# Kernel optimization log

Measured on AMD Instinct MI355X. Metric: run time of the kernel, lower is better.

The kernel has to match this reference:

```python
import jax, jax.numpy as jnp
import numpy as np
import math

B = 2
D_MODEL = 2048
L_MAX = 4096
FILTER_ORDER = 64
EMB_DIM = 3
SHORT_K = 3


def setup_inputs() -> dict:
    key = jax.random.key(0)
    ks = jax.random.split(key, 16)
    D = D_MODEL

    def n(k, shape, scale=0.02):
        return jax.random.normal(k, shape, dtype=jnp.float32) * scale

    return {
        "x": jax.random.normal(ks[0], (B, L_MAX, D), dtype=jnp.float32),
        "in_proj_w": n(ks[1], (3 * D, D)),
        "in_proj_b": n(ks[2], (3 * D,)),
        "short_w": n(ks[3], (3 * D, 1, SHORT_K), 0.3),   # depthwise conv weight (O, I/groups=1, K)
        "short_b": n(ks[4], (3 * D,), 0.1),
        "mlp_w0": n(ks[5], (FILTER_ORDER, EMB_DIM), 0.5),
        "mlp_b0": n(ks[6], (FILTER_ORDER,), 0.5),
        "sin_freq": jnp.ones((1, FILTER_ORDER), dtype=jnp.float32),  # Sin module, w=1, shared across MLP layers
        "mlp_w1": n(ks[7], (FILTER_ORDER, FILTER_ORDER), 0.1),
        "mlp_b1": n(ks[8], (FILTER_ORDER,), 0.1),
        "mlp_w2": n(ks[9], (FILTER_ORDER, FILTER_ORDER), 0.1),
        "mlp_b2": n(ks[10], (FILTER_ORDER,), 0.1),
        "mlp_w3": n(ks[11], (D, FILTER_ORDER), 0.1),      # final Linear(order -> d_model, bias=False)
        "filter_bias": jax.random.normal(ks[12], (D,), dtype=jnp.float32),  # HyenaFilter.bias ~ randn
        "out_proj_w": n(ks[13], (D, D)),
        "out_proj_b": n(ks[14], (D,)),
    }


def _pos_emb(L):
    # PositionalEmbedding: t in [0,1], 1 complex band (emb_dim=3 -> bands=1)
    t = jnp.linspace(0.0, 1.0, L)[:, None]               # (L, 1)
    t_resc = jnp.linspace(0.0, L - 1.0, L)
    w = 2.0 * math.pi * t_resc / L                       # (L,)
    bands = (EMB_DIM - 1) // 2
    f = jnp.linspace(1e-4, bands - 1.0, bands)           # (bands,)
    ang = f[None, :] * w[:, None]                        # (L, bands)
    # z = exp(-1j * f * w) -> real = cos, imag = -sin
    z = jnp.concatenate([t, jnp.cos(ang), -jnp.sin(ang)], axis=-1)  # (L, 3)
    return z, t


def _filter_k(L, w0, b0, freq, w1, b1, w2, b2, w3):
    z, t = _pos_emb(L)
    h = jnp.sin(freq * (z @ w0.T + b0))
    h = jnp.sin(freq * (h @ w1.T + b1))
    h = jnp.sin(freq * (h @ w2.T + b2))
    h = h @ w3.T                                         # (L, D)
    # ExponentialModulation: deltas = linspace(log(.01)/1.5, log(.01)/0.3, D)
    max_decay = math.log(0.01) / 0.3
    min_decay = math.log(0.01) / 1.5
    deltas = jnp.linspace(min_decay, max_decay, h.shape[-1])
    decay = jnp.exp(-t * jnp.abs(deltas)[None, :])       # (L, D)
    return (h * decay).T                                 # (D, L)


def _fftconv(u, k, bias):
    # fftconv_ref with gelu=False, no dropout_mask: u (B, D, L), k (D, L), bias (D,)
    L = u.shape[-1]
    n = 2 * L
    k_f = jnp.fft.rfft(k, n=n) / n                       # (D, L+1)
    u_f = jnp.fft.rfft(u, n=n)                           # (B, D, L+1)
    y = jnp.fft.irfft(u_f * k_f, n=n, norm="forward")[..., :L]
    return y + u * bias[:, None]


def reference(x, in_proj_w, in_proj_b, short_w, short_b, mlp_w0, mlp_b0, sin_freq,
              mlp_w1, mlp_b1, mlp_w2, mlp_b2, mlp_w3, filter_bias,
              out_proj_w, out_proj_b):
    Bn, L, D = x.shape
    u = x @ in_proj_w.T + in_proj_b                      # (B, L, 3D)
    u = jnp.transpose(u, (0, 2, 1))                      # (B, 3D, L)
    # depthwise short conv, padding = short_k - 1, truncate to L (causal-ish)
    uc = jax.lax.conv_general_dilated(
        u, short_w, window_strides=(1,),
        padding=[(SHORT_K - 1, SHORT_K - 1)],
        feature_group_count=3 * D,
        dimension_numbers=("NCH", "OIH", "NCH"))
    uc = uc[..., :L] + short_b[None, :, None]
    x0, x1, v = jnp.split(uc, 3, axis=1)                 # each (B, D, L)
    k = _filter_k(L, mlp_w0, mlp_b0, sin_freq, mlp_w1, mlp_b1, mlp_w2, mlp_b2, mlp_w3)
    # order=2 Hyena recurrence: single gated long-conv step
    v = v * x1
    v = _fftconv(v, k, filter_bias)
    y = v * x0                                           # (B, D, L)
    y = jnp.transpose(y, (0, 2, 1))                      # (B, L, D)
    return y @ out_proj_w.T + out_proj_b
```

## Files before the change

### kernel.cpp

```cpp
#include <hip/hip_runtime.h>
#include <hip/hip_bf16.h>
#include <cstdint>
#include <cstddef>

typedef __attribute__((ext_vector_type(8))) short    bf16x8;
typedef __attribute__((ext_vector_type(4))) float    f32x4;
typedef __attribute__((ext_vector_type(8))) unsigned short u16x8;
typedef __attribute__((ext_vector_type(4))) float    f32v4;
typedef __attribute__((ext_vector_type(4))) unsigned short u16v4;

__device__ __forceinline__ float b2f(unsigned short v) {
    return __builtin_bit_cast(float, ((unsigned int)v) << 16);
}
__device__ __forceinline__ unsigned short f2b(float f) {
    unsigned int u = __builtin_bit_cast(unsigned int, f);
    u += 0x7fffu + ((u >> 16) & 1u);
    return (unsigned short)(u >> 16);
}

__device__ __forceinline__ void async16(const void* g, void* l) {
    __builtin_amdgcn_global_load_lds(
        (const __attribute__((address_space(1))) unsigned int*)g,
        (__attribute__((address_space(3))) unsigned int*)l, 16, 0, 0);
}

__global__ __launch_bounds__(256) void cvt2_f32_bf16(
    const float* __restrict__ srcA, unsigned short* __restrict__ dstA, int n4A,
    const float* __restrict__ srcB, unsigned short* __restrict__ dstB, int n4B) {
    int i = blockIdx.x * blockDim.x + threadIdx.x;
    int stride = gridDim.x * blockDim.x;
    const int nTot = n4A + n4B;
    for (; i < nTot; i += stride) {
        const bool inA = (i < n4A);
        const f32v4* s4 = inA ? (const f32v4*)srcA : (const f32v4*)srcB;
        u16v4* d4 = inA ? (u16v4*)dstA : (u16v4*)dstB;
        const int k = inA ? i : (i - n4A);
        f32v4 v = s4[k];
        u16v4 o;
        o.x = f2b(v.x); o.y = f2b(v.y); o.z = f2b(v.z); o.w = f2b(v.w);
        d4[k] = o;
    }
}

__global__ __launch_bounds__(256) void cvt_f32_bf16(const float* __restrict__ src,
                                                    unsigned short* __restrict__ dst, int n4) {
    int i = blockIdx.x * blockDim.x + threadIdx.x;
    int stride = gridDim.x * blockDim.x;
    const f32v4* s4 = (const f32v4*)src;
    u16v4* d4 = (u16v4*)dst;
    for (; i < n4; i += stride) {
        f32v4 v = s4[i];
        u16v4 o;
        o.x = f2b(v.x); o.y = f2b(v.y); o.z = f2b(v.z); o.w = f2b(v.w);
        d4[i] = o;
    }
}

template <int MODE>
__global__ __launch_bounds__(512, 1) void gemm256(
    const unsigned short* __restrict__ A,
    const unsigned short* __restrict__ Bw,
    const float* __restrict__ bias,
    void* __restrict__ Cout,
    int M, int N, int K, int Lseq, int CH, int ntn)
{
    constexpr int SMEM_BYTES = (MODE == 1) ? 135168 : 131072;
    __shared__ char smemc[SMEM_BYTES];

    const int tid = threadIdx.x;
    const int w   = tid >> 6;
    const int l   = tid & 63;
    const int wm  = w & 1;
    const int wn  = w >> 1;
    const int quad = l >> 4;
    const int lq   = l & 15;

    const int bid = blockIdx.x;
    const int x  = bid & 7;
    const int j  = bid >> 3;
    const int bx = (j & 7) + 8 * (j >> 5);
    const int by = (x << 2) | ((j >> 3) & 3);
    const int n0 = bx * 256, m0 = by * 256;

    const int su0 = quad ^ (lq & 7);
    const int su1 = su0 ^ 4;

    uint32_t offAe[2][2], offBe[2][2];
    int dA[2][2], dB[2][2];
    #pragma unroll
    for (int h = 0; h < 2; ++h)
        #pragma unroll
        for (int c = 0; c < 2; ++c) {
            const int Lr = h * 128 + w * 16 + c * 8 + (l >> 3);
            const int gA = ((Lr & 64) << 1) | ((Lr & 128) >> 1) | (Lr & 63);
            const int u  = (l & 7) ^ (l >> 3);
            offAe[h][c] = (uint32_t)(m0 + gA) * (uint32_t)K + (uint32_t)(u * 8);
            offBe[h][c] = (uint32_t)(n0 + Lr) * (uint32_t)K + (uint32_t)(u * 8);
            const int rb = (h * 128 + w * 16 + c * 8) * 128;
            dA[h][c] = rb;
            dB[h][c] = 32768 + rb;
        }

#define STAGE_A(bs, h, tile) do { \
    async16(A + offAe[h][0] + (size_t)(tile) * 64, smemc + ((bs) * 65536 + dA[h][0])); \
    async16(A + offAe[h][1] + (size_t)(tile) * 64, smemc + ((bs) * 65536 + dA[h][1])); \
} while (0)
#define STAGE_B(bs, h, tile) do { \
    async16(Bw + offBe[h][0] + (size_t)(tile) * 64, smemc + ((bs) * 65536 + dB[h][0])); \
    async16(Bw + offBe[h][1] + (size_t)(tile) * 64, smemc + ((bs) * 65536 + dB[h][1])); \
} while (0)

    f32x4 acc[8][4] = {};
    bf16x8 bw[4][2], a[2][2];

#define LDB8(bs) do { \
    _Pragma("unroll") for (int jj = 0; jj < 4; ++jj) { \
        const int Lr = wn * 64 + jj * 16 + lq; \
        bw[jj][0] = *(const bf16x8*)(smemc + (bs) * 65536 + 32768 + Lr * 128 + su0 * 16); \
        bw[jj][1] = *(const bf16x8*)(smemc + (bs) * 65536 + 32768 + Lr * 128 + su1 * 16); \
    } } while (0)
#define LDA4(bs, q) do { \
    _Pragma("unroll") for (int mf = 0; mf < 2; ++mf) { \
        const int g = wm * 128 + (q) * 32 + mf * 16 + lq; \
        const int Lr = ((g & 64) << 1) | ((g & 128) >> 1) | (g & 63); \
        a[mf][0] = *(const bf16x8*)(smemc + (bs) * 65536 + Lr * 128 + su0 * 16); \
        a[mf][1] = *(const bf16x8*)(smemc + (bs) * 65536 + Lr * 128 + su1 * 16); \
    } } while (0)
#define MFMA16(q) do { \
    _Pragma("unroll") for (int mf = 0; mf < 2; ++mf) \
    _Pragma("unroll") for (int jj = 0; jj < 4; ++jj) \
    _Pragma("unroll") for (int kk = 0; kk < 2; ++kk) \
        acc[(q) * 2 + mf][jj] = __builtin_amdgcn_mfma_f32_16x16x32_bf16(a[mf][kk], bw[jj][kk], acc[(q) * 2 + mf][jj], 0, 0, 0); \
} while (0)
#define PHASE_SYNC() do { \
    __builtin_amdgcn_s_barrier(); \
    asm volatile("s_waitcnt lgkmcnt(0)" ::: "memory"); \
    __builtin_amdgcn_sched_barrier(0); \
    __builtin_amdgcn_s_setprio(1); \
} while (0)
#define PHASE_END() do { \
    __builtin_amdgcn_s_setprio(0); \
    __builtin_amdgcn_s_barrier(); \
} while (0)
#define PHASE_END_DRAIN(lastf) do { \
    __builtin_amdgcn_s_setprio(0); \
    if (lastf) asm volatile("s_waitcnt vmcnt(0)" ::: "memory"); \
    else       asm volatile("s_waitcnt vmcnt(6)" ::: "memory"); \
    __builtin_amdgcn_s_barrier(); \
} while (0)

    STAGE_B(0, 0, 0); STAGE_B(0, 1, 0); STAGE_A(0, 0, 0); STAGE_A(0, 1, 0);
    STAGE_B(1, 0, 1); STAGE_B(1, 1, 1); STAGE_A(1, 0, 1);
    asm volatile("s_waitcnt vmcnt(6)" ::: "memory");
    __builtin_amdgcn_s_barrier();

    const int nIt = K >> 7;
    for (int i = 0; i < nIt; ++i) {
        const bool last = (i == nIt - 1);
        const int t0 = 2 * i, t1 = 2 * i + 1;
        LDB8(0); LDA4(0, 0); STAGE_A(1, 1, t1);
        PHASE_SYNC(); MFMA16(0); PHASE_END();
        LDA4(0, 1); if (!last) STAGE_B(0, 0, t0 + 2);
        PHASE_SYNC(); MFMA16(1); PHASE_END();
        LDA4(0, 2); if (!last) STAGE_B(0, 1, t0 + 2);
        PHASE_SYNC(); MFMA16(2); PHASE_END();
        LDA4(0, 3); if (!last) STAGE_A(0, 0, t0 + 2);
        PHASE_SYNC(); MFMA16(3); PHASE_END_DRAIN(last);
        LDB8(1); LDA4(1, 0); if (!last) STAGE_A(0, 1, t0 + 2);
        PHASE_SYNC(); MFMA16(0); PHASE_END();
        LDA4(1, 1); if (!last) STAGE_B(1, 0, t1 + 2);
        PHASE_SYNC(); MFMA16(1); PHASE_END();
        LDA4(1, 2); if (!last) STAGE_B(1, 1, t1 + 2);
        PHASE_SYNC(); MFMA16(2); PHASE_END();
        LDA4(1, 3); if (!last) STAGE_A(1, 0, t1 + 2);
        PHASE_SYNC(); MFMA16(3); PHASE_END_DRAIN(last);
    }

    if (MODE == 0) {
        float* out = (float*)Cout;
        #pragma unroll
        for (int jj = 0; jj < 4; ++jj) {
            const int col = n0 + wn * 64 + jj * 16 + lq;
            const float bv = bias[col];
            #pragma unroll
            for (int i8 = 0; i8 < 8; ++i8) {
                const int rowb = m0 + wm * 128 + i8 * 16 + quad * 4;
                f32x4 c = acc[i8][jj];
                out[(size_t)(rowb + 0) * N + col] = c.x + bv;
                out[(size_t)(rowb + 1) * N + col] = c.y + bv;
                out[(size_t)(rowb + 2) * N + col] = c.z + bv;
                out[(size_t)(rowb + 3) * N + col] = c.w + bv;
            }
        }
    } else {
        unsigned short* sE = (unsigned short*)smemc;
        __syncthreads();
        #pragma unroll
        for (int jj = 0; jj < 4; ++jj) {
            const int nl = wn * 64 + jj * 16 + lq;
            const float bv = bias[n0 + nl];
            #pragma unroll
            for (int i8 = 0; i8 < 8; ++i8) {
                const int ml = wm * 128 + i8 * 16 + quad * 4;
                f32x4 c = acc[i8][jj];
                u16v4 pk;
                pk.x = f2b(c.x + bv); pk.y = f2b(c.y + bv);
                pk.z = f2b(c.z + bv); pk.w = f2b(c.w + bv);
                *(u16v4*)&sE[nl * 264 + ml] = pk;
            }
        }
        __syncthreads();
        unsigned short* uo = (unsigned short*)Cout;
        const int bI = m0 >> 12;
        const int l0 = m0 & 4095;
        for (int e = tid; e < 8192; e += 512) {
            const int nl = e >> 5, seg = e & 31;
            u16x8 v = *(const u16x8*)&sE[nl * 264 + seg * 8];
            *(u16x8*)&uo[(size_t)(bI * CH + n0 + nl) * Lseq + l0 + seg * 8] = v;
        }
    }
#undef STAGE_A
#undef STAGE_B
#undef LDB8
#undef LDA4
#undef MFMA16
#undef PHASE_SYNC
#undef PHASE_END
#undef PHASE_END_DRAIN
}

__global__ __launch_bounds__(256) void filter_kernel(
    const float* __restrict__ w0, const float* __restrict__ b0,
    const float* __restrict__ freq,
    const float* __restrict__ w1, const float* __restrict__ b1,
    const float* __restrict__ w2, const float* __restrict__ b2,
    const float* __restrict__ w3, float* __restrict__ kf)
{
    __shared__ float ha[64][64];
    __shared__ float hb[64][64];
    const int tid = threadIdx.x;
    const int l0 = blockIdx.x * 64;
    const int d0 = blockIdx.y * 256;
    const int l  = tid & 63;
    const int lg = l0 + l;
    const float tt = (float)lg * (1.0f / 4095.0f);
    const float wang = 6.283185307179586f * (float)lg * (1.0f / 4096.0f);
    const float a  = 1e-4f * wang;
    const float z0 = tt, z1 = cosf(a), z2 = -sinf(a);

    for (int e = tid; e < 4096; e += 256) {
        const int dim = e >> 6;
        float pre = z0 * w0[dim * 3] + z1 * w0[dim * 3 + 1] + z2 * w0[dim * 3 + 2] + b0[dim];
        ha[dim][l] = sinf(freq[dim] * pre);
    }
    __syncthreads();
    for (int e = tid; e < 4096; e += 256) {
        const int dim = e >> 6;
        float acc = b1[dim];
        #pragma unroll
        for (int jj = 0; jj < 64; ++jj) acc += w1[dim * 64 + jj] * ha[jj][l];
        hb[dim][l] = sinf(freq[dim] * acc);
    }
    __syncthreads();
    for (int e = tid; e < 4096; e += 256) {
        const int dim = e >> 6;
        float acc = b2[dim];
        #pragma unroll
        for (int jj = 0; jj < 64; ++jj) acc += w2[dim * 64 + jj] * hb[jj][l];
        ha[dim][l] = sinf(freq[dim] * acc);
    }
    __syncthreads();
    for (int d = d0 + (tid >> 6); d < d0 + 256; d += 4) {
        float acc = 0.f;
        #pragma unroll
        for (int jj = 0; jj < 64; ++jj) acc += w3[d * 64 + jj] * ha[jj][l];
        const float delta = fabsf(-3.0701134573253944f + (-5.999245642062483e-3f) * (float)d);
        kf[(size_t)d * 4096 + lg] = acc * __expf(-tt * delta);
    }
}

#define PIDX(i) ((i) + (((i) >> 5) << 2))

__device__ __forceinline__ void bfly_f(float& r1, float& i1, float& r2, float& i2, float wr, float wi) {
    float ur = r1, ui = i1, vr = r2, vi = i2;
    r1 = ur + vr; i1 = ui + vi;
    float dr = ur - vr, di = ui - vi;
    r2 = dr * wr - di * wi;
    i2 = dr * wi + di * wr;
}
__device__ __forceinline__ void bfly_i(float& r1, float& i1, float& r2, float& i2, float wr, float wi) {
    float vr = r2 * wr - i2 * wi, vi = r2 * wi + i2 * wr;
    float ur = r1, ui = i1;
    r1 = ur + vr; i1 = ui + vi;
    r2 = ur - vr; i2 = ui - vi;
}

template <int DS, int STR>
__device__ __forceinline__ void fwd_stage(float* re, float* im, int tt) {
    float wr[8], wi[8];
    constexpr float c = -3.14159265358979f / (float)(STR * DS);
    #pragma unroll
    for (int k = 0; k < DS; ++k) __sincosf(c * (float)(tt + STR * k), &wi[k], &wr[k]);
    #pragma unroll
    for (int s = 0; s < 16; ++s)
        if ((s & DS) == 0)
            bfly_f(re[s], im[s], re[s + DS], im[s + DS], wr[s & (DS - 1)], wi[s & (DS - 1)]);
}
template <int DS, int STR>
__device__ __forceinline__ void inv_stage(float* re, float* im, int tt) {
    float wr[8], wi[8];
    constexpr float c = 3.14159265358979f / (float)(STR * DS);
    #pragma unroll
    for (int k = 0; k < DS; ++k) __sincosf(c * (float)(tt + STR * k), &wi[k], &wr[k]);
    #pragma unroll
    for (int s = 0; s < 16; ++s)
        if ((s & DS) == 0)
            bfly_i(re[s], im[s], re[s + DS], im[s + DS], wr[s & (DS - 1)], wi[s & (DS - 1)]);
}

__device__ constexpr float TW8C[8] = { 1.f,  0.9238795325112867f,  0.7071067811865476f,  0.3826834323650898f,
                                       0.f, -0.3826834323650898f, -0.7071067811865476f, -0.9238795325112867f };
__device__ constexpr float TW8S[8] = { 0.f,  0.3826834323650898f,  0.7071067811865476f,  0.9238795325112867f,
                                       1.f,  0.9238795325112867f,  0.7071067811865476f,  0.3826834323650898f };
template <int DS>
__device__ __forceinline__ void fwd_stageC(float* re, float* im) {
    #pragma unroll
    for (int s = 0; s < 16; ++s)
        if ((s & DS) == 0) {
            const int k = (s & (DS - 1)) * (8 / DS);
            bfly_f(re[s], im[s], re[s + DS], im[s + DS], TW8C[k], -TW8S[k]);
        }
}
template <int DS>
__device__ __forceinline__ void inv_stageC(float* re, float* im) {
    #pragma unroll
    for (int s = 0; s < 16; ++s)
        if ((s & DS) == 0) {
            const int k = (s & (DS - 1)) * (8 / DS);
            bfly_i(re[s], im[s], re[s + DS], im[s + DS], TW8C[k], TW8S[k]);
        }
}

__device__ __forceinline__ void xchg(float* re, float* im, float* fre, float* fim,
                                     int wbase, int wstr, int rbase, int rstr) {
    __syncthreads();
    if (wstr == 1) {
        #pragma unroll
        for (int q = 0; q < 4; ++q) {
            f32x4 vr, vi;
            vr.x = re[4*q+0]; vr.y = re[4*q+1]; vr.z = re[4*q+2]; vr.w = re[4*q+3];
            vi.x = im[4*q+0]; vi.y = im[4*q+1]; vi.z = im[4*q+2]; vi.w = im[4*q+3];
            *(f32x4*)&fre[PIDX(wbase + 4*q)] = vr;
            *(f32x4*)&fim[PIDX(wbase + 4*q)] = vi;
        }
    } else {
        #pragma unroll
        for (int s = 0; s < 16; ++s) {
            const int i = wbase + wstr * s;
            fre[PIDX(i)] = re[s]; fim[PIDX(i)] = im[s];
        }
    }
    __syncthreads();
    if (rstr == 1) {
        #pragma unroll
        for (int q = 0; q < 4; ++q) {
            f32x4 vr = *(const f32x4*)&fre[PIDX(rbase + 4*q)];
            f32x4 vi = *(const f32x4*)&fim[PIDX(rbase + 4*q)];
            re[4*q+0] = vr.x; re[4*q+1] = vr.y; re[4*q+2] = vr.z; re[4*q+3] = vr.w;
            im[4*q+0] = vi.x; im[4*q+1] = vi.y; im[4*q+2] = vi.z; im[4*q+3] = vi.w;
        }
    } else {
        #pragma unroll
        for (int s = 0; s < 16; ++s) {
            const int i = rbase + rstr * s;
            re[s] = fre[PIDX(i)]; im[s] = fim[PIDX(i)];
        }
    }
}

__device__ __forceinline__ void fwd_fft(float* re, float* im, float* fre, float* fim, int t) {
    const int off = t & 31, seg = t >> 5;
    fwd_stage<8, 512>(re, im, t);
    fwd_stage<4, 512>(re, im, t);
    fwd_stage<2, 512>(re, im, t);
    fwd_stage<1, 512>(re, im, t);
    xchg(re, im, fre, fim, t, 512, seg * 512 + off, 32);
    fwd_stage<8, 32>(re, im, off);
    fwd_stage<4, 32>(re, im, off);
    fwd_stage<2, 32>(re, im, off);
    fwd_stage<1, 32>(re, im, off);
    {
        float wr, wi;
        __sincosf(-3.14159265358979f * (float)(off & 15) / 16.0f, &wi, &wr);
        const bool hi = (off & 16) != 0;
        #pragma unroll
        for (int s = 0; s < 16; ++s) {
            float rr = __shfl_xor(re[s], 16);
            float ri = __shfl_xor(im[s], 16);
            if (!hi) { re[s] += rr; im[s] += ri; }
            else {
                float dr = rr - re[s], di = ri - im[s];
                re[s] = dr * wr - di * wi;
                im[s] = dr * wi + di * wr;
            }
        }
    }
    xchg(re, im, fre, fim, seg * 512 + off, 32, 16 * t, 1);
    fwd_stageC<8>(re, im);
    fwd_stageC<4>(re, im);
    fwd_stageC<2>(re, im);
    fwd_stageC<1>(re, im);
}

__device__ __forceinline__ void inv_fft(float* re, float* im, float* fre, float* fim, int t) {
    const int off = t & 31, seg = t >> 5;
    inv_stageC<1>(re, im);
    inv_stageC<2>(re, im);
    inv_stageC<4>(re, im);
    inv_stageC<8>(re, im);
    xchg(re, im, fre, fim, 16 * t, 1, seg * 512 + off, 32);
    {
        float wr, wi;
        __sincosf(3.14159265358979f * (float)(off & 15) / 16.0f, &wi, &wr);
        const bool hi = (off & 16) != 0;
        #pragma unroll
        for (int s = 0; s < 16; ++s) {
            float rr = __shfl_xor(re[s], 16);
            float ri = __shfl_xor(im[s], 16);
            if (!hi) {
                float vr = rr * wr - ri * wi, vi = rr * wi + ri * wr;
                re[s] += vr; im[s] += vi;
            } else {
                float vr = re[s] * wr - im[s] * wi, vi = re[s] * wi + im[s] * wr;
                re[s] = rr - vr; im[s] = ri - vi;
            }
        }
    }
    inv_stage<1, 32>(re, im, off);
    inv_stage<2, 32>(re, im, off);
    inv_stage<4, 32>(re, im, off);
    inv_stage<8, 32>(re, im, off);
    xchg(re, im, fre, fim, seg * 512 + off, 32, t, 512);
    inv_stage<1, 512>(re, im, t);
    inv_stage<2, 512>(re, im, t);
    inv_stage<4, 512>(re, im, t);
    inv_stage<8, 512>(re, im, t);
}

__global__ __launch_bounds__(512, 2) void kfft_kernel(
    const float* __restrict__ kf,
    float* __restrict__ kspec)
{
    __shared__ __align__(16) float fre[9216];
    __shared__ __align__(16) float fim[9216];
    const int t = threadIdx.x;
    const int d = blockIdx.x;
    float kr[16], ki[16];
    #pragma unroll
    for (int s = 0; s < 16; ++s) {
        kr[s] = (s < 8) ? kf[(size_t)d * 4096 + t + 512 * s] : 0.f;
        ki[s] = 0.f;
    }
    fwd_fft(kr, ki, fre, fim, t);
    f32x4* kv = (f32x4*)kspec + (size_t)d * 4096 + t;
    #pragma unroll
    for (int q = 0; q < 8; ++q) {
        f32x4 o;
        o.x = kr[2 * q]; o.y = ki[2 * q];
        o.z = kr[2 * q + 1]; o.w = ki[2 * q + 1];
        kv[q * 512] = o;
    }
}

__device__ __forceinline__ void conv8(const unsigned short* __restrict__ row, int lb,
                                      float W0, float W1, float W2, float BB,
                                      float* __restrict__ out) {
    u16x8 v8 = *(const u16x8*)(row + lb);
    float f[8];
    #pragma unroll
    for (int j = 0; j < 8; ++j) f[j] = b2f(v8[j]);
    const float fm1 = (lb >= 1) ? b2f(row[lb - 1]) : 0.f;
    const float fm2 = (lb >= 2) ? b2f(row[lb - 2]) : 0.f;
    out[0] = W0 * fm2 + W1 * fm1 + W2 * f[0] + BB;
    out[1] = W0 * fm1 + W1 * f[0] + W2 * f[1] + BB;
    #pragma unroll
    for (int j = 2; j < 8; ++j) out[j] = W0 * f[j - 2] + W1 * f[j - 1] + W2 * f[j] + BB;
}

__global__ __launch_bounds__(512, 2) void hyena_fft_kernel(
    const unsigned short* __restrict__ u,
    const float* __restrict__ kspec,
    const float* __restrict__ sw,
    const float* __restrict__ sbv,
    const float* __restrict__ fbias,
    unsigned short* __restrict__ zb)
{
    __shared__ __align__(16) float fre[9216];
    __shared__ __align__(16) float fim[9216];
    const int t = threadIdx.x;
    const int d = blockIdx.x;
    const int lb = t << 3;

    const int c0 = d, c1 = 2048 + d, c2 = 4096 + d;
    const float w00 = sw[c0*3+0], w01 = sw[c0*3+1], w02 = sw[c0*3+2], bb0 = sbv[c0];
    const float w10 = sw[c1*3+0], w11 = sw[c1*3+1], w12 = sw[c1*3+2], bb1 = sbv[c1];
    const float w20 = sw[c2*3+0], w21 = sw[c2*3+1], w22 = sw[c2*3+2], bb2 = sbv[c2];
    const float fb = fbias[d];

    float vgc[2][8], x0c[2][8];
    #pragma unroll
    for (int b = 0; b < 2; ++b) {
        const size_t base = (size_t)b * 6144 * 4096;
        float a_[8], e_[8], g_[8];
        conv8(u + base + (size_t)c0 * 4096, lb, w00, w01, w02, bb0, a_);
        conv8(u + base + (size_t)c1 * 4096, lb, w10, w11, w12, bb1, e_);
        conv8(u + base + (size_t)c2 * 4096, lb, w20, w21, w22, bb2, g_);
        #pragma unroll
        for (int j = 0; j < 8; ++j) { x0c[b][j] = a_[j]; vgc[b][j] = g_[j] * e_[j]; }
    }

    #pragma unroll
    for (int q = 0; q < 2; ++q) {
        f32x4 vr, vi;
        vr.x = vgc[0][4*q+0]; vr.y = vgc[0][4*q+1]; vr.z = vgc[0][4*q+2]; vr.w = vgc[0][4*q+3];
        vi.x = vgc[1][4*q+0]; vi.y = vgc[1][4*q+1]; vi.z = vgc[1][4*q+2]; vi.w = vgc[1][4*q+3];
        *(f32x4*)&fre[PIDX(lb + 4*q)] = vr;
        *(f32x4*)&fim[PIDX(lb + 4*q)] = vi;
    }
    __syncthreads();
    float xr[16], xi[16];
    #pragma unroll
    for (int s = 0; s < 8; ++s) {
        xr[s] = fre[PIDX(t + (s << 9))];
        xi[s] = fim[PIDX(t + (s << 9))];
    }
    #pragma unroll
    for (int s = 8; s < 16; ++s) { xr[s] = 0.f; xi[s] = 0.f; }

    fwd_fft(xr, xi, fre, fim, t);
    {
        const f32x4* kv = (const f32x4*)kspec + (size_t)d * 4096 + t;
        f32x4 kk[8];
        #pragma unroll
        for (int q = 0; q < 8; ++q) kk[q] = kv[q * 512];
        #pragma unroll
        for (int q = 0; q < 8; ++q) {
            float cr = xr[2 * q], ci = xi[2 * q];
            xr[2 * q] = cr * kk[q].x - ci * kk[q].y;
            xi[2 * q] = cr * kk[q].y + ci * kk[q].x;
            cr = xr[2 * q + 1]; ci = xi[2 * q + 1];
            xr[2 * q + 1] = cr * kk[q].z - ci * kk[q].w;
            xi[2 * q + 1] = cr * kk[q].w + ci * kk[q].z;
        }
    }
    inv_fft(xr, xi, fre, fim, t);

    __syncthreads();
    #pragma unroll
    for (int s = 0; s < 8; ++s) {
        fre[PIDX(t + (s << 9))] = xr[s];
        fim[PIDX(t + (s << 9))] = xi[s];
    }
    __syncthreads();
    float yr[8], yi[8];
    #pragma unroll
    for (int q = 0; q < 2; ++q) {
        f32x4 vr = *(const f32x4*)&fre[PIDX(lb + 4*q)];
        f32x4 vi = *(const f32x4*)&fim[PIDX(lb + 4*q)];
        yr[4*q+0] = vr.x; yr[4*q+1] = vr.y; yr[4*q+2] = vr.z; yr[4*q+3] = vr.w;
        yi[4*q+0] = vi.x; yi[4*q+1] = vi.y; yi[4*q+2] = vi.z; yi[4*q+3] = vi.w;
    }
    const float inv_n = 1.0f / 8192.0f;
    u16x8 z0v, z1v;
    #pragma unroll
    for (int j = 0; j < 8; ++j) {
        z0v[j] = (unsigned short)f2b((yr[j] * inv_n + vgc[0][j] * fb) * x0c[0][j]);
        z1v[j] = (unsigned short)f2b((yi[j] * inv_n + vgc[1][j] * fb) * x0c[1][j]);
    }
    *(u16x8*)&zb[(size_t)d * 4096 + lb]          = z0v;
    *(u16x8*)&zb[(size_t)(2048 + d) * 4096 + lb] = z1v;
}

__global__ __launch_bounds__(256) void transpose_kernel(const unsigned short* __restrict__ zb,
                                                        unsigned short* __restrict__ zt)
{
    __shared__ unsigned int tile[64][65];
    const int l0 = blockIdx.x * 64, d0 = blockIdx.y * 64, b = blockIdx.z;
    const int tid = threadIdx.x;
    for (int e = tid; e < 4096; e += 256) {
        const int r = e >> 6, c = e & 63;
        tile[r][c] = zb[(size_t)(b * 2048 + d0 + r) * 4096 + l0 + c];
    }
    __syncthreads();
    for (int e = tid; e < 4096; e += 256) {
        const int r = e >> 6, c = e & 63;
        zt[(size_t)(b * 4096 + l0 + r) * 2048 + d0 + c] = (unsigned short)tile[c][r];
    }
}

extern "C" void kernel_launch(void* const* d_in, const int* in_sizes, int n_in,
                              void* d_out, int out_size, void* d_ws, size_t ws_size,
                              hipStream_t stream)
{
    const float* x   = (const float*)d_in[0];
    const float* ipw = (const float*)d_in[1];
    const float* ipb = (const float*)d_in[2];
    const float* sw  = (const float*)d_in[3];
    const float* sb  = (const float*)d_in[4];
    const float* w0  = (const float*)d_in[5];
    const float* b0  = (const float*)d_in[6];
    const float* fr  = (const float*)d_in[7];
    const float* w1  = (const float*)d_in[8];
    const float* b1  = (const float*)d_in[9];
    const float* w2  = (const float*)d_in[10];
    const float* b2  = (const float*)d_in[11];
    const float* w3  = (const float*)d_in[12];
    const float* fb  = (const float*)d_in[13];
    const float* opw = (const float*)d_in[14];
    const float* opb = (const float*)d_in[15];
    float* out = (float*)d_out;

    char* ws = (char*)d_ws;
    unsigned short* xb    = (unsigned short*)ws;
    unsigned short* wbi   = (unsigned short*)(ws + 33554432);
    float*          kspec = (float*)ws;
    unsigned short* ztb   = (unsigned short*)ws;
    unsigned short* wbo   = (unsigned short*)(ws + 33554432);
    unsigned short* ub    = (unsigned short*)(ws + 134217728);
    float*          kf    = (float*)(ws + 234881024);
    unsigned short* zbm   = (unsigned short*)(ws + 234881024);

    cvt2_f32_bf16<<<1536, 256, 0, stream>>>(x, xb, 16777216 / 4, ipw, wbi, 12582912 / 4);

    gemm256<1><<<768, 512, 0, stream>>>(xb, wbi, ipb, ub, 8192, 6144, 2048, 4096, 6144, 24);

    filter_kernel<<<dim3(64, 8), 256, 0, stream>>>(w0, b0, fr, w1, b1, w2, b2, w3, kf);

    kfft_kernel<<<2048, 512, 0, stream>>>(kf, kspec);

    hyena_fft_kernel<<<2048, 512, 0, stream>>>(ub, kspec, sw, sb, fb, zbm);

    transpose_kernel<<<dim3(64, 32, 2), 256, 0, stream>>>(zbm, ztb);

    cvt_f32_bf16<<<512,  256, 0, stream>>>(opw, wbo, 4194304 / 4);

    gemm256<0><<<256, 512, 0, stream>>>(ztb, wbo, opb, out, 8192, 2048, 2048, 4096, 2048, 8);
}
```

Measured before the change: 733.3 us.

## Fuse filter FFT into hyena conv kernel and prefetch conv inputs early

Drops the separate kfft kernel. Each hyena block now computes the filter spectrum in registers with its own forward FFT, which removes the kspec round trip through global memory (2048×4096×16 bytes written then read). Loads of the short-conv inputs are issued early so their latency overlaps the filter FFT, and the x0 loads overlap the inverse FFT. The cost is an extra FFT per block, higher register pressure, and a workspace layout change.

```diff
diff --git a/kernel.cpp b/kernel.cpp
--- a/kernel.cpp
+++ b/kernel.cpp
@@ -447,49 +447,29 @@
     inv_stage<8, 512>(re, im, t);
 }
 
-__global__ __launch_bounds__(512, 2) void kfft_kernel(
-    const float* __restrict__ kf,
-    float* __restrict__ kspec)
-{
-    __shared__ __align__(16) float fre[9216];
-    __shared__ __align__(16) float fim[9216];
-    const int t = threadIdx.x;
-    const int d = blockIdx.x;
-    float kr[16], ki[16];
-    #pragma unroll
-    for (int s = 0; s < 16; ++s) {
-        kr[s] = (s < 8) ? kf[(size_t)d * 4096 + t + 512 * s] : 0.f;
-        ki[s] = 0.f;
-    }
-    fwd_fft(kr, ki, fre, fim, t);
-    f32x4* kv = (f32x4*)kspec + (size_t)d * 4096 + t;
-    #pragma unroll
-    for (int q = 0; q < 8; ++q) {
-        f32x4 o;
-        o.x = kr[2 * q]; o.y = ki[2 * q];
-        o.z = kr[2 * q + 1]; o.w = ki[2 * q + 1];
-        kv[q * 512] = o;
-    }
-}
-
-__device__ __forceinline__ void conv8(const unsigned short* __restrict__ row, int lb,
-                                      float W0, float W1, float W2, float BB,
-                                      float* __restrict__ out) {
-    u16x8 v8 = *(const u16x8*)(row + lb);
+struct ConvPre { u16x8 v; float m1, m2; };
+__device__ __forceinline__ ConvPre conv_pre(const unsigned short* __restrict__ row, int lb) {
+    ConvPre p;
+    p.v  = *(const u16x8*)(row + lb);
+    p.m1 = (lb >= 1) ? b2f(row[lb - 1]) : 0.f;
+    p.m2 = (lb >= 2) ? b2f(row[lb - 2]) : 0.f;
+    return p;
+}
+__device__ __forceinline__ void conv_do(const ConvPre& p,
+                                        float W0, float W1, float W2, float BB,
+                                        float* __restrict__ out) {
     float f[8];
     #pragma unroll
-    for (int j = 0; j < 8; ++j) f[j] = b2f(v8[j]);
-    const float fm1 = (lb >= 1) ? b2f(row[lb - 1]) : 0.f;
-    const float fm2 = (lb >= 2) ? b2f(row[lb - 2]) : 0.f;
-    out[0] = W0 * fm2 + W1 * fm1 + W2 * f[0] + BB;
-    out[1] = W0 * fm1 + W1 * f[0] + W2 * f[1] + BB;
+    for (int j = 0; j < 8; ++j) f[j] = b2f((unsigned short)p.v[j]);
+    out[0] = W0 * p.m2 + W1 * p.m1 + W2 * f[0] + BB;
+    out[1] = W0 * p.m1 + W1 * f[0] + W2 * f[1] + BB;
     #pragma unroll
     for (int j = 2; j < 8; ++j) out[j] = W0 * f[j - 2] + W1 * f[j - 1] + W2 * f[j] + BB;
 }
 
 __global__ __launch_bounds__(512, 2) void hyena_fft_kernel(
     const unsigned short* __restrict__ u,
-    const float* __restrict__ kspec,
+    const float* __restrict__ kf,
     const float* __restrict__ sw,
     const float* __restrict__ sbv,
     const float* __restrict__ fbias,
@@ -502,23 +482,37 @@
     const int lb = t << 3;
 
     const int c0 = d, c1 = 2048 + d, c2 = 4096 + d;
-    const float w00 = sw[c0*3+0], w01 = sw[c0*3+1], w02 = sw[c0*3+2], bb0 = sbv[c0];
     const float w10 = sw[c1*3+0], w11 = sw[c1*3+1], w12 = sw[c1*3+2], bb1 = sbv[c1];
     const float w20 = sw[c2*3+0], w21 = sw[c2*3+1], w22 = sw[c2*3+2], bb2 = sbv[c2];
     const float fb = fbias[d];
 
-    float vgc[2][8], x0c[2][8];
+    ConvPre p1[2], p2[2];
     #pragma unroll
     for (int b = 0; b < 2; ++b) {
         const size_t base = (size_t)b * 6144 * 4096;
-        float a_[8], e_[8], g_[8];
-        conv8(u + base + (size_t)c0 * 4096, lb, w00, w01, w02, bb0, a_);
-        conv8(u + base + (size_t)c1 * 4096, lb, w10, w11, w12, bb1, e_);
-        conv8(u + base + (size_t)c2 * 4096, lb, w20, w21, w22, bb2, g_);
-        #pragma unroll
-        for (int j = 0; j < 8; ++j) { x0c[b][j] = a_[j]; vgc[b][j] = g_[j] * e_[j]; }
-    }
-
+        p1[b] = conv_pre(u + base + (size_t)c1 * 4096, lb);
+        p2[b] = conv_pre(u + base + (size_t)c2 * 4096, lb);
+    }
+
+    float kr[16], ki[16];
+    #pragma unroll
+    for (int s = 0; s < 16; ++s) {
+        kr[s] = (s < 8) ? kf[(size_t)d * 4096 + t + 512 * s] : 0.f;
+        ki[s] = 0.f;
+    }
+    fwd_fft(kr, ki, fre, fim, t);
+
+    float vgc[2][8];
+    #pragma unroll
+    for (int b = 0; b < 2; ++b) {
+        float e_[8], g_[8];
+        conv_do(p1[b], w10, w11, w12, bb1, e_);
+        conv_do(p2[b], w20, w21, w22, bb2, g_);
+        #pragma unroll
+        for (int j = 0; j < 8; ++j) vgc[b][j] = g_[j] * e_[j];
+    }
+
+    __syncthreads();
     #pragma unroll
     for (int q = 0; q < 2; ++q) {
         f32x4 vr, vi;
@@ -538,21 +532,18 @@
     for (int s = 8; s < 16; ++s) { xr[s] = 0.f; xi[s] = 0.f; }
 
     fwd_fft(xr, xi, fre, fim, t);
-    {
-        const f32x4* kv = (const f32x4*)kspec + (size_t)d * 4096 + t;
-        f32x4 kk[8];
-        #pragma unroll
-        for (int q = 0; q < 8; ++q) kk[q] = kv[q * 512];
-        #pragma unroll
-        for (int q = 0; q < 8; ++q) {
-            float cr = xr[2 * q], ci = xi[2 * q];
-            xr[2 * q] = cr * kk[q].x - ci * kk[q].y;
-            xi[2 * q] = cr * kk[q].y + ci * kk[q].x;
-            cr = xr[2 * q + 1]; ci = xi[2 * q + 1];
-            xr[2 * q + 1] = cr * kk[q].z - ci * kk[q].w;
-            xi[2 * q + 1] = cr * kk[q].w + ci * kk[q].z;
-        }
-    }
+    #pragma unroll
+    for (int j = 0; j < 16; ++j) {
+        const float cr = xr[j], ci = xi[j];
+        xr[j] = cr * kr[j] - ci * ki[j];
+        xi[j] = cr * ki[j] + ci * kr[j];
+    }
+
+    ConvPre p0[2];
+    #pragma unroll
+    for (int b = 0; b < 2; ++b)
+        p0[b] = conv_pre(u + (size_t)b * 6144 * 4096 + (size_t)c0 * 4096, lb);
+
     inv_fft(xr, xi, fre, fim, t);
 
     __syncthreads();
@@ -570,15 +561,19 @@
         yr[4*q+0] = vr.x; yr[4*q+1] = vr.y; yr[4*q+2] = vr.z; yr[4*q+3] = vr.w;
         yi[4*q+0] = vi.x; yi[4*q+1] = vi.y; yi[4*q+2] = vi.z; yi[4*q+3] = vi.w;
     }
+    const float w00 = sw[c0*3+0], w01 = sw[c0*3+1], w02 = sw[c0*3+2], bb0 = sbv[c0];
     const float inv_n = 1.0f / 8192.0f;
-    u16x8 z0v, z1v;
-    #pragma unroll
-    for (int j = 0; j < 8; ++j) {
-        z0v[j] = (unsigned short)f2b((yr[j] * inv_n + vgc[0][j] * fb) * x0c[0][j]);
-        z1v[j] = (unsigned short)f2b((yi[j] * inv_n + vgc[1][j] * fb) * x0c[1][j]);
-    }
-    *(u16x8*)&zb[(size_t)d * 4096 + lb]          = z0v;
-    *(u16x8*)&zb[(size_t)(2048 + d) * 4096 + lb] = z1v;
+    #pragma unroll
+    for (int b = 0; b < 2; ++b) {
+        float a_[8];
+        conv_do(p0[b], w00, w01, w02, bb0, a_);
+        const float* Y = (b == 0) ? yr : yi;
+        u16x8 zv;
+        #pragma unroll
+        for (int j = 0; j < 8; ++j)
+            zv[j] = (unsigned short)f2b((Y[j] * inv_n + vgc[b][j] * fb) * a_[j]);
+        *(u16x8*)&zb[(size_t)(b * 2048 + d) * 4096 + lb] = zv;
+    }
 }
 
 __global__ __launch_bounds__(256) void transpose_kernel(const unsigned short* __restrict__ zb,
@@ -621,14 +616,13 @@
     float* out = (float*)d_out;
 
     char* ws = (char*)d_ws;
-    unsigned short* xb    = (unsigned short*)ws;
-    unsigned short* wbi   = (unsigned short*)(ws + 33554432);
-    float*          kspec = (float*)ws;
-    unsigned short* ztb   = (unsigned short*)ws;
-    unsigned short* wbo   = (unsigned short*)(ws + 33554432);
-    unsigned short* ub    = (unsigned short*)(ws + 134217728);
-    float*          kf    = (float*)(ws + 234881024);
-    unsigned short* zbm   = (unsigned short*)(ws + 234881024);
+    unsigned short* xb  = (unsigned short*)ws;
+    unsigned short* wbi = (unsigned short*)(ws + 33554432);
+    unsigned short* zbm = (unsigned short*)ws;
+    unsigned short* ztb = (unsigned short*)(ws + 33554432);
+    unsigned short* wbo = (unsigned short*)(ws + 67108864);
+    unsigned short* ub  = (unsigned short*)(ws + 134217728);
+    float*          kf  = (float*)(ws + 234881024);
 
     cvt2_f32_bf16<<<1536, 256, 0, stream>>>(x, xb, 16777216 / 4, ipw, wbi, 12582912 / 4);
 
@@ -636,13 +630,11 @@
 
     filter_kernel<<<dim3(64, 8), 256, 0, stream>>>(w0, b0, fr, w1, b1, w2, b2, w3, kf);
 
-    kfft_kernel<<<2048, 512, 0, stream>>>(kf, kspec);
-
-    hyena_fft_kernel<<<2048, 512, 0, stream>>>(ub, kspec, sw, sb, fb, zbm);
+    cvt_f32_bf16<<<512, 256, 0, stream>>>(opw, wbo, 4194304 / 4);
+
+    hyena_fft_kernel<<<2048, 512, 0, stream>>>(ub, kf, sw, sb, fb, zbm);
 
     transpose_kernel<<<dim3(64, 32, 2), 256, 0, stream>>>(zbm, ztb);
 
-    cvt_f32_bf16<<<512,  256, 0, stream>>>(opw, wbo, 4194304 / 4);
-
     gemm256<0><<<256, 512, 0, stream>>>(ztb, wbo, opb, out, 8192, 2048, 2048, 4096, 2048, 8);
 }
```

Result: no change. 737.0 us (+0.5%).
